# Kernel optimization log

Hardware: AMD Instinct MI355X
Metric: run time of the kernel (lower is better)

The kernel has to match this reference:

```python
import jax, jax.numpy as jnp
import numpy as np

B, C, D, H, W = 2, 128, 16, 16, 16

def setup_inputs() -> dict:
    key = jax.random.key(0)
    ks = jax.random.split(key, 7)
    s = 0.02
    return {
        "x": jax.random.normal(ks[0], (B, C, D, H, W), jnp.float32),
        "Wq": jax.random.normal(ks[1], (C, C), jnp.float32) * s,
        "bq": jax.random.normal(ks[2], (C,), jnp.float32) * s,
        "Wk": jax.random.normal(ks[3], (C, C), jnp.float32) * s,
        "bk": jax.random.normal(ks[4], (C,), jnp.float32) * s,
        "Wv": jax.random.normal(ks[5], (C, C), jnp.float32) * s,
        "bv": jax.random.normal(ks[6], (C,), jnp.float32) * s,
    }

def reference(x, Wq, bq, Wk, bk, Wv, bv):
    b, c, d, h, w = x.shape
    n = d * h * w
    xf = x.reshape(b, c, n)  # [B, C, N]
    # 1x1x1 Conv3d == per-voxel linear over channels
    q = jnp.einsum('oc,bcn->bon', Wq, xf) + bq[None, :, None]
    k = jnp.einsum('oc,bcn->bon', Wk, xf) + bk[None, :, None]
    v = jnp.einsum('oc,bcn->bon', Wv, xf) + bv[None, :, None]
    # energy[b,n,m] = sum_c q[b,c,n] * k[b,c,m]  (no scale, as in source)
    energy = jnp.einsum('bcn,bcm->bnm', q, k)
    attention = jax.nn.softmax(energy, axis=-1)
    # out[b,c,n] = sum_m v[b,c,m] * attention[b,n,m]
    out = jnp.einsum('bcm,bnm->bcn', v, attention)
    return out.reshape(b, c, d, h, w)
```

## Files before the change

### kernel.cpp

```cpp
#include <hip/hip_runtime.h>


typedef __bf16 bf16x8 __attribute__((ext_vector_type(8)));
typedef float  f32x4  __attribute__((ext_vector_type(4)));
typedef unsigned short ushort8 __attribute__((ext_vector_type(8)));
typedef unsigned short ushort4v __attribute__((ext_vector_type(4)));

#define LDP 136
#define LDV 72
#define LDO 133

constexpr int CB = 128;
constexpr int NB = 4096;
constexpr int BB = 2;

__device__ __forceinline__ unsigned short f2bf(float f) {
  union { float f; unsigned int i; } v; v.f = f;
  unsigned int x = v.i;
  return (unsigned short)((x + 0x7fffu + ((x >> 16) & 1u)) >> 16);
}
__device__ __forceinline__ bf16x8 ldfrag(const unsigned short* lds, int row, int koff, int ld) {
  return *(const bf16x8*)(lds + row * ld + koff);
}

__global__ __launch_bounds__(256) void qkv_proj_kernel(
    const float* __restrict__ x,
    const float* __restrict__ Wq, const float* __restrict__ bq,
    const float* __restrict__ Wk, const float* __restrict__ bk,
    const float* __restrict__ Wv, const float* __restrict__ bv,
    unsigned short* __restrict__ Qt, unsigned short* __restrict__ Kt,
    unsigned short* __restrict__ Vo)
{
  extern __shared__ __align__(16) char smem_raw[];
  unsigned short* xT = (unsigned short*)smem_raw;
  unsigned short* Wl = xT + 64 * LDP;

  const int b  = blockIdx.y;
  const int n0 = blockIdx.x * 64;
  const int m  = blockIdx.z;
  const int t  = threadIdx.x;
  const int lane = t & 63, w = t >> 6;
  const int l15 = lane & 15, quad = lane >> 4;

  const float* W = (m == 0) ? Wq : (m == 1) ? Wk : Wv;
  const float* bias_p = (m == 0) ? bq : (m == 1) ? bk : bv;

  for (int v = t; v < 2048; v += 256) {
    int c = v >> 4, i4 = v & 15;
    float4 d = *(const float4*)(x + (b * CB + c) * NB + n0 + i4 * 4);
    xT[(i4 * 4 + 0) * LDP + c] = f2bf(d.x);
    xT[(i4 * 4 + 1) * LDP + c] = f2bf(d.y);
    xT[(i4 * 4 + 2) * LDP + c] = f2bf(d.z);
    xT[(i4 * 4 + 3) * LDP + c] = f2bf(d.w);
  }
  for (int v = t; v < 4096; v += 256) {
    int o = v >> 5, c4 = v & 31;
    float4 d = *(const float4*)(W + o * 128 + c4 * 4);
    ushort4v u = {f2bf(d.x), f2bf(d.y), f2bf(d.z), f2bf(d.w)};
    *(ushort4v*)(Wl + o * LDP + c4 * 4) = u;
  }
  __syncthreads();

  if (m < 2) {
    f32x4 acc[8];
#pragma unroll
    for (int ct = 0; ct < 8; ct++) acc[ct] = (f32x4)0.0f;
#pragma unroll
    for (int ks = 0; ks < 4; ks++) {
      int koff = ks * 32 + quad * 8;
      bf16x8 a = ldfrag(xT, w * 16 + l15, koff, LDP);
#pragma unroll
      for (int ct = 0; ct < 8; ct++) {
        bf16x8 bb = ldfrag(Wl, ct * 16 + l15, koff, LDP);
        acc[ct] = __builtin_amdgcn_mfma_f32_16x16x32_bf16(a, bb, acc[ct], 0, 0, 0);
      }
    }
    unsigned short* O = (m == 0) ? Qt : Kt;
#pragma unroll
    for (int ct = 0; ct < 8; ct++) {
      int o = ct * 16 + l15;
      float bias = bias_p[o];
#pragma unroll
      for (int r = 0; r < 4; r++) {
        int i = w * 16 + quad * 4 + r;
        O[(b * NB + n0 + i) * CB + o] = f2bf(acc[ct][r] + bias);
      }
    }
  } else {
    f32x4 acc[2][4];
#pragma unroll
    for (int rr = 0; rr < 2; rr++)
#pragma unroll
      for (int ct = 0; ct < 4; ct++) acc[rr][ct] = (f32x4)0.0f;
#pragma unroll
    for (int ks = 0; ks < 4; ks++) {
      int koff = ks * 32 + quad * 8;
      bf16x8 a0 = ldfrag(Wl, (w * 2 + 0) * 16 + l15, koff, LDP);
      bf16x8 a1 = ldfrag(Wl, (w * 2 + 1) * 16 + l15, koff, LDP);
#pragma unroll
      for (int ct = 0; ct < 4; ct++) {
        bf16x8 bb = ldfrag(xT, ct * 16 + l15, koff, LDP);
        acc[0][ct] = __builtin_amdgcn_mfma_f32_16x16x32_bf16(a0, bb, acc[0][ct], 0, 0, 0);
        acc[1][ct] = __builtin_amdgcn_mfma_f32_16x16x32_bf16(a1, bb, acc[1][ct], 0, 0, 0);
      }
    }
#pragma unroll
    for (int rr = 0; rr < 2; rr++)
#pragma unroll
      for (int ct = 0; ct < 4; ct++)
#pragma unroll
        for (int r = 0; r < 4; r++) {
          int o = (w * 2 + rr) * 16 + quad * 4 + r;
          int i = ct * 16 + l15;
          Vo[(b * CB + o) * NB + n0 + i] = f2bf(acc[rr][ct][r] + bias_p[o]);
        }
  }
}

__global__ __launch_bounds__(512, 4) void attn_part_kernel(
    const unsigned short* __restrict__ Qt,
    const unsigned short* __restrict__ Kt,
    const unsigned short* __restrict__ Vo,
    float* __restrict__ Opart, float* __restrict__ Ll, int ksz)
{
  extern __shared__ __align__(16) char smem_raw[];
  unsigned short* Kl = (unsigned short*)smem_raw;
  unsigned short* Vl = Kl + 64 * LDP;
  unsigned short* Pl = Vl + 128 * LDV;

  const int b  = blockIdx.y;
  const int q0 = blockIdx.x * 128;
  const int s  = blockIdx.z;
  const int k_base = s * ksz;
  const int nit = ksz >> 6;
  const int t  = threadIdx.x;
  const int lane = t & 63, w = t >> 6;
  const int l15 = lane & 15, quad = lane >> 4;

  bf16x8 qf[4];
#pragma unroll
  for (int ks = 0; ks < 4; ks++)
    qf[ks] = *(const bf16x8*)(Qt + ((size_t)(b * NB + q0 + w * 16 + l15)) * CB +
                              ks * 32 + quad * 8);

  for (int v = t; v < 1024; v += 512) {
    int j = v >> 4, c8 = v & 15;
    *(ushort8*)(Kl + j * LDP + c8 * 8) =
        *(const ushort8*)(Kt + (size_t)(b * NB + k_base + j) * CB + c8 * 8);
  }
  for (int v = t; v < 1024; v += 512) {
    int c = v >> 3, j8 = v & 7;
    *(ushort8*)(Vl + c * LDV + j8 * 8) =
        *(const ushort8*)(Vo + (size_t)(b * CB + c) * NB + k_base + j8 * 8);
  }

  float lsum[4] = {0.0f, 0.0f, 0.0f, 0.0f};
  f32x4 o_acc[8];
#pragma unroll
  for (int tt = 0; tt < 8; tt++) o_acc[tt] = (f32x4)0.0f;

  __syncthreads();

  for (int it = 0; it < nit; it++) {
    ushort8 kr[2], vr[2];
    if (it + 1 < nit) {
      int m1 = k_base + (it + 1) * 64;
#pragma unroll
      for (int u = 0; u < 2; u++) {
        int v = t + u * 512;
        int j = v >> 4, c8 = v & 15;
        kr[u] = *(const ushort8*)(Kt + (size_t)(b * NB + m1 + j) * CB + c8 * 8);
      }
#pragma unroll
      for (int u = 0; u < 2; u++) {
        int v = t + u * 512;
        int c = v >> 3, j8 = v & 7;
        vr[u] = *(const ushort8*)(Vo + (size_t)(b * CB + c) * NB + m1 + j8 * 8);
      }
    }

    f32x4 sacc[4];
#pragma unroll
    for (int tt = 0; tt < 4; tt++) sacc[tt] = (f32x4)0.0f;
#pragma unroll
    for (int ks = 0; ks < 4; ks++) {
      int koff = ks * 32 + quad * 8;
#pragma unroll
      for (int tt = 0; tt < 4; tt++) {
        bf16x8 bb = ldfrag(Kl, tt * 16 + l15, koff, LDP);
        sacc[tt] = __builtin_amdgcn_mfma_f32_16x16x32_bf16(qf[ks], bb, sacc[tt], 0, 0, 0);
      }
    }

#pragma unroll
    for (int tt = 0; tt < 4; tt++) {
#pragma unroll
      for (int r = 0; r < 4; r++) {
        float p = __expf(sacc[tt][r]);
        sacc[tt][r] = p;
        lsum[r] += p;
        Pl[(w * 16 + quad * 4 + r) * LDV + tt * 16 + l15] = f2bf(p);
      }
    }
    asm volatile("s_waitcnt lgkmcnt(0)" ::: "memory");

#pragma unroll
    for (int ks = 0; ks < 2; ks++) {
      int koff = ks * 32 + quad * 8;
      bf16x8 a = ldfrag(Pl, w * 16 + l15, koff, LDV);
#pragma unroll
      for (int tt = 0; tt < 8; tt++) {
        bf16x8 bb = ldfrag(Vl, tt * 16 + l15, koff, LDV);
        o_acc[tt] = __builtin_amdgcn_mfma_f32_16x16x32_bf16(a, bb, o_acc[tt], 0, 0, 0);
      }
    }

    if (it + 1 < nit) {
      __syncthreads();
#pragma unroll
      for (int u = 0; u < 2; u++) {
        int v = t + u * 512;
        int j = v >> 4, c8 = v & 15;
        *(ushort8*)(Kl + j * LDP + c8 * 8) = kr[u];
      }
#pragma unroll
      for (int u = 0; u < 2; u++) {
        int v = t + u * 512;
        int c = v >> 3, j8 = v & 7;
        *(ushort8*)(Vl + c * LDV + j8 * 8) = vr[u];
      }
      __syncthreads();
    }
  }

#pragma unroll
  for (int r = 0; r < 4; r++) {
    lsum[r] += __shfl_xor(lsum[r], 1, 16);
    lsum[r] += __shfl_xor(lsum[r], 2, 16);
    lsum[r] += __shfl_xor(lsum[r], 4, 16);
    lsum[r] += __shfl_xor(lsum[r], 8, 16);
  }

  const size_t obase = ((size_t)(s * BB + b) * NB + q0) * CB;
#pragma unroll
  for (int tt = 0; tt < 8; tt++)
#pragma unroll
    for (int r = 0; r < 4; r++)
      Opart[obase + (size_t)(w * 16 + quad * 4 + r) * CB + tt * 16 + l15] = o_acc[tt][r];
  if (l15 == 0) {
    const size_t lbase = (size_t)(s * BB + b) * NB + q0 + w * 16;
#pragma unroll
    for (int r = 0; r < 4; r++) Ll[lbase + quad * 4 + r] = lsum[r];
  }
}

__global__ __launch_bounds__(256) void combine_kernel(
    const float* __restrict__ Opart, const float* __restrict__ Ll,
    float* __restrict__ out, int nsplit)
{
  extern __shared__ __align__(16) char smem_raw[];
  float* Olf = (float*)smem_raw;

  const int b  = blockIdx.y;
  const int n0 = blockIdx.x * 64;
  const int t  = threadIdx.x;
  const int i  = t >> 2;
  const int c0 = (t & 3) * 32;

  float L = 0.0f;
  for (int s = 0; s < nsplit; s++)
    L += Ll[(size_t)(s * BB + b) * NB + n0 + i];

  f32x4 acc[8];
#pragma unroll
  for (int u = 0; u < 8; u++) acc[u] = (f32x4)0.0f;
  for (int s = 0; s < nsplit; s++) {
    const float* src = Opart + ((size_t)(s * BB + b) * NB + n0 + i) * CB + c0;
#pragma unroll
    for (int u = 0; u < 8; u++) acc[u] += *(const f32x4*)(src + u * 4);
  }
  float invL = 1.0f / L;
#pragma unroll
  for (int u = 0; u < 8; u++) {
    acc[u] *= invL;
    *(f32x4*)(Olf + i * LDO + c0 + u * 4) = acc[u];
  }
  __syncthreads();

  for (int v = t; v < 2048; v += 256) {
    int c = v >> 4, i4 = v & 15;
    float4 d;
    d.x = Olf[(i4 * 4 + 0) * LDO + c];
    d.y = Olf[(i4 * 4 + 1) * LDO + c];
    d.z = Olf[(i4 * 4 + 2) * LDO + c];
    d.w = Olf[(i4 * 4 + 3) * LDO + c];
    *(float4*)(out + (size_t)(b * CB + c) * NB + n0 + i4 * 4) = d;
  }
}

extern "C" void kernel_launch(void* const* d_in, const int* in_sizes, int n_in,
                              void* d_out, int out_size, void* d_ws, size_t ws_size,
                              hipStream_t stream) {
  const float* x  = (const float*)d_in[0];
  const float* Wq = (const float*)d_in[1];
  const float* bq = (const float*)d_in[2];
  const float* Wk = (const float*)d_in[3];
  const float* bk = (const float*)d_in[4];
  const float* Wv = (const float*)d_in[5];
  const float* bv = (const float*)d_in[6];
  float* out = (float*)d_out;

  const size_t qkv_elems = (size_t)BB * NB * CB;
  unsigned short* Qt = (unsigned short*)d_ws;
  unsigned short* Kt = Qt + qkv_elems;
  unsigned short* Vo = Kt + qkv_elems;
  char* ws_tail = (char*)(Vo + qkv_elems);
  size_t tail_sz = ws_size - 3 * qkv_elems * sizeof(unsigned short);

  const size_t per_split = (size_t)BB * NB * CB * 4 + (size_t)BB * NB * 4;
  int nsplit = 8;
  while (nsplit > 1 && (size_t)nsplit * per_split > tail_sz) nsplit >>= 1;

  float* Opart = (float*)ws_tail;
  float* Ll    = Opart + (size_t)nsplit * BB * NB * CB;
  const int ksz = NB / nsplit;

  const int qkv_smem  = (64 * LDP + 128 * LDP) * 2;
  const int attn_smem = (64 * LDP + 128 * LDV + 128 * LDV) * 2;
  const int comb_smem = 64 * LDO * 4;

  qkv_proj_kernel<<<dim3(NB / 64, BB, 3), 256, qkv_smem, stream>>>(
      x, Wq, bq, Wk, bk, Wv, bv, Qt, Kt, Vo);
  attn_part_kernel<<<dim3(NB / 128, BB, nsplit), 512, attn_smem, stream>>>(
      Qt, Kt, Vo, Opart, Ll, ksz);
  combine_kernel<<<dim3(NB / 64, BB), 256, comb_smem, stream>>>(
      Opart, Ll, out, nsplit);
}
```

Baseline: 125.6 us.

## Use 32-row query tiles per wave, split combine over channels, native bf16 casts

The attention kernel now runs 4 waves of 256 threads, each handling two 16-row query subtiles. Every K/V fragment read from LDS therefore feeds two MFMAs, halving LDS traffic per FLOP, at the cost of more accumulator registers. The combine kernel is split into four channel groups so it launches four times as many blocks, with a smaller LDS transpose tile. Manual float-to-bf16 rounding is replaced with native __bf16 casts, which may lower to hardware conversion instructions.

```diff
diff --git a/kernel.cpp b/kernel.cpp
--- a/kernel.cpp
+++ b/kernel.cpp
@@ -2,24 +2,18 @@
 
 
 typedef __bf16 bf16x8 __attribute__((ext_vector_type(8)));
+typedef __bf16 bf16x4v __attribute__((ext_vector_type(4)));
 typedef float  f32x4  __attribute__((ext_vector_type(4)));
-typedef unsigned short ushort8 __attribute__((ext_vector_type(8)));
-typedef unsigned short ushort4v __attribute__((ext_vector_type(4)));
 
 #define LDP 136
 #define LDV 72
-#define LDO 133
+#define LDO 33
 
 constexpr int CB = 128;
 constexpr int NB = 4096;
 constexpr int BB = 2;
 
-__device__ __forceinline__ unsigned short f2bf(float f) {
-  union { float f; unsigned int i; } v; v.f = f;
-  unsigned int x = v.i;
-  return (unsigned short)((x + 0x7fffu + ((x >> 16) & 1u)) >> 16);
-}
-__device__ __forceinline__ bf16x8 ldfrag(const unsigned short* lds, int row, int koff, int ld) {
+__device__ __forceinline__ bf16x8 ldfrag(const __bf16* lds, int row, int koff, int ld) {
   return *(const bf16x8*)(lds + row * ld + koff);
 }
 
@@ -28,12 +22,11 @@
     const float* __restrict__ Wq, const float* __restrict__ bq,
     const float* __restrict__ Wk, const float* __restrict__ bk,
     const float* __restrict__ Wv, const float* __restrict__ bv,
-    unsigned short* __restrict__ Qt, unsigned short* __restrict__ Kt,
-    unsigned short* __restrict__ Vo)
+    __bf16* __restrict__ Qt, __bf16* __restrict__ Kt, __bf16* __restrict__ Vo)
 {
   extern __shared__ __align__(16) char smem_raw[];
-  unsigned short* xT = (unsigned short*)smem_raw;
-  unsigned short* Wl = xT + 64 * LDP;
+  __bf16* xT = (__bf16*)smem_raw;
+  __bf16* Wl = xT + 64 * LDP;
 
   const int b  = blockIdx.y;
   const int n0 = blockIdx.x * 64;
@@ -48,16 +41,16 @@
   for (int v = t; v < 2048; v += 256) {
     int c = v >> 4, i4 = v & 15;
     float4 d = *(const float4*)(x + (b * CB + c) * NB + n0 + i4 * 4);
-    xT[(i4 * 4 + 0) * LDP + c] = f2bf(d.x);
-    xT[(i4 * 4 + 1) * LDP + c] = f2bf(d.y);
-    xT[(i4 * 4 + 2) * LDP + c] = f2bf(d.z);
-    xT[(i4 * 4 + 3) * LDP + c] = f2bf(d.w);
+    xT[(i4 * 4 + 0) * LDP + c] = (__bf16)d.x;
+    xT[(i4 * 4 + 1) * LDP + c] = (__bf16)d.y;
+    xT[(i4 * 4 + 2) * LDP + c] = (__bf16)d.z;
+    xT[(i4 * 4 + 3) * LDP + c] = (__bf16)d.w;
   }
   for (int v = t; v < 4096; v += 256) {
     int o = v >> 5, c4 = v & 31;
     float4 d = *(const float4*)(W + o * 128 + c4 * 4);
-    ushort4v u = {f2bf(d.x), f2bf(d.y), f2bf(d.z), f2bf(d.w)};
-    *(ushort4v*)(Wl + o * LDP + c4 * 4) = u;
+    bf16x4v u = {(__bf16)d.x, (__bf16)d.y, (__bf16)d.z, (__bf16)d.w};
+    *(bf16x4v*)(Wl + o * LDP + c4 * 4) = u;
   }
   __syncthreads();
 
@@ -75,7 +68,7 @@
         acc[ct] = __builtin_amdgcn_mfma_f32_16x16x32_bf16(a, bb, acc[ct], 0, 0, 0);
       }
     }
-    unsigned short* O = (m == 0) ? Qt : Kt;
+    __bf16* O = (m == 0) ? Qt : Kt;
 #pragma unroll
     for (int ct = 0; ct < 8; ct++) {
       int o = ct * 16 + l15;
@@ -83,7 +76,7 @@
 #pragma unroll
       for (int r = 0; r < 4; r++) {
         int i = w * 16 + quad * 4 + r;
-        O[(b * NB + n0 + i) * CB + o] = f2bf(acc[ct][r] + bias);
+        O[(b * NB + n0 + i) * CB + o] = (__bf16)(acc[ct][r] + bias);
       }
     }
   } else {
@@ -112,21 +105,21 @@
         for (int r = 0; r < 4; r++) {
           int o = (w * 2 + rr) * 16 + quad * 4 + r;
           int i = ct * 16 + l15;
-          Vo[(b * CB + o) * NB + n0 + i] = f2bf(acc[rr][ct][r] + bias_p[o]);
+          Vo[(b * CB + o) * NB + n0 + i] = (__bf16)(acc[rr][ct][r] + bias_p[o]);
         }
   }
 }
 
-__global__ __launch_bounds__(512, 4) void attn_part_kernel(
-    const unsigned short* __restrict__ Qt,
-    const unsigned short* __restrict__ Kt,
-    const unsigned short* __restrict__ Vo,
+__global__ __launch_bounds__(256, 2) void attn_part_kernel(
+    const __bf16* __restrict__ Qt,
+    const __bf16* __restrict__ Kt,
+    const __bf16* __restrict__ Vo,
     float* __restrict__ Opart, float* __restrict__ Ll, int ksz)
 {
   extern __shared__ __align__(16) char smem_raw[];
-  unsigned short* Kl = (unsigned short*)smem_raw;
-  unsigned short* Vl = Kl + 64 * LDP;
-  unsigned short* Pl = Vl + 128 * LDV;
+  __bf16* Kl = (__bf16*)smem_raw;
+  __bf16* Vl = Kl + 64 * LDP;
+  __bf16* Pl = Vl + 128 * LDV;
 
   const int b  = blockIdx.y;
   const int q0 = blockIdx.x * 128;
@@ -136,121 +129,143 @@
   const int t  = threadIdx.x;
   const int lane = t & 63, w = t >> 6;
   const int l15 = lane & 15, quad = lane >> 4;
-
-  bf16x8 qf[4];
-#pragma unroll
-  for (int ks = 0; ks < 4; ks++)
-    qf[ks] = *(const bf16x8*)(Qt + ((size_t)(b * NB + q0 + w * 16 + l15)) * CB +
-                              ks * 32 + quad * 8);
-
-  for (int v = t; v < 1024; v += 512) {
+  const int row0 = w * 32;
+
+  bf16x8 qf[2][4];
+#pragma unroll
+  for (int st = 0; st < 2; st++)
+#pragma unroll
+    for (int ks = 0; ks < 4; ks++)
+      qf[st][ks] = *(const bf16x8*)(Qt +
+          (size_t)(b * NB + q0 + row0 + st * 16 + l15) * CB + ks * 32 + quad * 8);
+
+#pragma unroll
+  for (int u = 0; u < 4; u++) {
+    int v = t + u * 256;
     int j = v >> 4, c8 = v & 15;
-    *(ushort8*)(Kl + j * LDP + c8 * 8) =
-        *(const ushort8*)(Kt + (size_t)(b * NB + k_base + j) * CB + c8 * 8);
-  }
-  for (int v = t; v < 1024; v += 512) {
+    *(bf16x8*)(Kl + j * LDP + c8 * 8) =
+        *(const bf16x8*)(Kt + (size_t)(b * NB + k_base + j) * CB + c8 * 8);
+  }
+#pragma unroll
+  for (int u = 0; u < 4; u++) {
+    int v = t + u * 256;
     int c = v >> 3, j8 = v & 7;
-    *(ushort8*)(Vl + c * LDV + j8 * 8) =
-        *(const ushort8*)(Vo + (size_t)(b * CB + c) * NB + k_base + j8 * 8);
-  }
-
-  float lsum[4] = {0.0f, 0.0f, 0.0f, 0.0f};
-  f32x4 o_acc[8];
-#pragma unroll
-  for (int tt = 0; tt < 8; tt++) o_acc[tt] = (f32x4)0.0f;
+    *(bf16x8*)(Vl + c * LDV + j8 * 8) =
+        *(const bf16x8*)(Vo + (size_t)(b * CB + c) * NB + k_base + j8 * 8);
+  }
+
+  float lsum[2][4] = {{0, 0, 0, 0}, {0, 0, 0, 0}};
+  f32x4 o_acc[2][8];
+#pragma unroll
+  for (int st = 0; st < 2; st++)
+#pragma unroll
+    for (int tt = 0; tt < 8; tt++) o_acc[st][tt] = (f32x4)0.0f;
 
   __syncthreads();
 
   for (int it = 0; it < nit; it++) {
-    ushort8 kr[2], vr[2];
+    bf16x8 kr[4], vr[4];
     if (it + 1 < nit) {
       int m1 = k_base + (it + 1) * 64;
 #pragma unroll
-      for (int u = 0; u < 2; u++) {
-        int v = t + u * 512;
+      for (int u = 0; u < 4; u++) {
+        int v = t + u * 256;
         int j = v >> 4, c8 = v & 15;
-        kr[u] = *(const ushort8*)(Kt + (size_t)(b * NB + m1 + j) * CB + c8 * 8);
-      }
-#pragma unroll
-      for (int u = 0; u < 2; u++) {
-        int v = t + u * 512;
+        kr[u] = *(const bf16x8*)(Kt + (size_t)(b * NB + m1 + j) * CB + c8 * 8);
+      }
+#pragma unroll
+      for (int u = 0; u < 4; u++) {
+        int v = t + u * 256;
         int c = v >> 3, j8 = v & 7;
-        vr[u] = *(const ushort8*)(Vo + (size_t)(b * CB + c) * NB + m1 + j8 * 8);
-      }
-    }
-
-    f32x4 sacc[4];
-#pragma unroll
-    for (int tt = 0; tt < 4; tt++) sacc[tt] = (f32x4)0.0f;
+        vr[u] = *(const bf16x8*)(Vo + (size_t)(b * CB + c) * NB + m1 + j8 * 8);
+      }
+    }
+
+    f32x4 sacc[2][4];
+#pragma unroll
+    for (int st = 0; st < 2; st++)
+#pragma unroll
+      for (int tt = 0; tt < 4; tt++) sacc[st][tt] = (f32x4)0.0f;
 #pragma unroll
     for (int ks = 0; ks < 4; ks++) {
       int koff = ks * 32 + quad * 8;
 #pragma unroll
       for (int tt = 0; tt < 4; tt++) {
         bf16x8 bb = ldfrag(Kl, tt * 16 + l15, koff, LDP);
-        sacc[tt] = __builtin_amdgcn_mfma_f32_16x16x32_bf16(qf[ks], bb, sacc[tt], 0, 0, 0);
-      }
-    }
-
-#pragma unroll
-    for (int tt = 0; tt < 4; tt++) {
-#pragma unroll
-      for (int r = 0; r < 4; r++) {
-        float p = __expf(sacc[tt][r]);
-        sacc[tt][r] = p;
-        lsum[r] += p;
-        Pl[(w * 16 + quad * 4 + r) * LDV + tt * 16 + l15] = f2bf(p);
-      }
-    }
+        sacc[0][tt] = __builtin_amdgcn_mfma_f32_16x16x32_bf16(qf[0][ks], bb, sacc[0][tt], 0, 0, 0);
+        sacc[1][tt] = __builtin_amdgcn_mfma_f32_16x16x32_bf16(qf[1][ks], bb, sacc[1][tt], 0, 0, 0);
+      }
+    }
+
+#pragma unroll
+    for (int st = 0; st < 2; st++)
+#pragma unroll
+      for (int tt = 0; tt < 4; tt++)
+#pragma unroll
+        for (int r = 0; r < 4; r++) {
+          float p = __expf(sacc[st][tt][r]);
+          lsum[st][r] += p;
+          Pl[(row0 + st * 16 + quad * 4 + r) * LDV + tt * 16 + l15] = (__bf16)p;
+        }
     asm volatile("s_waitcnt lgkmcnt(0)" ::: "memory");
 
 #pragma unroll
     for (int ks = 0; ks < 2; ks++) {
       int koff = ks * 32 + quad * 8;
-      bf16x8 a = ldfrag(Pl, w * 16 + l15, koff, LDV);
+      bf16x8 a0 = ldfrag(Pl, row0 + l15, koff, LDV);
+      bf16x8 a1 = ldfrag(Pl, row0 + 16 + l15, koff, LDV);
 #pragma unroll
       for (int tt = 0; tt < 8; tt++) {
         bf16x8 bb = ldfrag(Vl, tt * 16 + l15, koff, LDV);
-        o_acc[tt] = __builtin_amdgcn_mfma_f32_16x16x32_bf16(a, bb, o_acc[tt], 0, 0, 0);
+        o_acc[0][tt] = __builtin_amdgcn_mfma_f32_16x16x32_bf16(a0, bb, o_acc[0][tt], 0, 0, 0);
+        o_acc[1][tt] = __builtin_amdgcn_mfma_f32_16x16x32_bf16(a1, bb, o_acc[1][tt], 0, 0, 0);
       }
     }
 
     if (it + 1 < nit) {
       __syncthreads();
 #pragma unroll
-      for (int u = 0; u < 2; u++) {
-        int v = t + u * 512;
+      for (int u = 0; u < 4; u++) {
+        int v = t + u * 256;
         int j = v >> 4, c8 = v & 15;
-        *(ushort8*)(Kl + j * LDP + c8 * 8) = kr[u];
-      }
-#pragma unroll
-      for (int u = 0; u < 2; u++) {
-        int v = t + u * 512;
+        *(bf16x8*)(Kl + j * LDP + c8 * 8) = kr[u];
+      }
+#pragma unroll
+      for (int u = 0; u < 4; u++) {
+        int v = t + u * 256;
         int c = v >> 3, j8 = v & 7;
-        *(ushort8*)(Vl + c * LDV + j8 * 8) = vr[u];
+        *(bf16x8*)(Vl + c * LDV + j8 * 8) = vr[u];
       }
       __syncthreads();
     }
   }
 
 #pragma unroll
-  for (int r = 0; r < 4; r++) {
-    lsum[r] += __shfl_xor(lsum[r], 1, 16);
-    lsum[r] += __shfl_xor(lsum[r], 2, 16);
-    lsum[r] += __shfl_xor(lsum[r], 4, 16);
-    lsum[r] += __shfl_xor(lsum[r], 8, 16);
-  }
+  for (int st = 0; st < 2; st++)
+#pragma unroll
+    for (int r = 0; r < 4; r++) {
+      lsum[st][r] += __shfl_xor(lsum[st][r], 1, 16);
+      lsum[st][r] += __shfl_xor(lsum[st][r], 2, 16);
+      lsum[st][r] += __shfl_xor(lsum[st][r], 4, 16);
+      lsum[st][r] += __shfl_xor(lsum[st][r], 8, 16);
+    }
 
   const size_t obase = ((size_t)(s * BB + b) * NB + q0) * CB;
 #pragma unroll
-  for (int tt = 0; tt < 8; tt++)
-#pragma unroll
-    for (int r = 0; r < 4; r++)
-      Opart[obase + (size_t)(w * 16 + quad * 4 + r) * CB + tt * 16 + l15] = o_acc[tt][r];
+  for (int st = 0; st < 2; st++)
+#pragma unroll
+    for (int tt = 0; tt < 8; tt++)
+#pragma unroll
+      for (int r = 0; r < 4; r++)
+        Opart[obase + (size_t)(row0 + st * 16 + quad * 4 + r) * CB + tt * 16 + l15] =
+            o_acc[st][tt][r];
   if (l15 == 0) {
-    const size_t lbase = (size_t)(s * BB + b) * NB + q0 + w * 16;
-#pragma unroll
-    for (int r = 0; r < 4; r++) Ll[lbase + quad * 4 + r] = lsum[r];
+    const size_t lbase = (size_t)(s * BB + b) * NB + q0 + row0;
+#pragma unroll
+    for (int st = 0; st < 2; st++)
+#pragma unroll
+      for (int r = 0; r < 4; r++)
+        Ll[lbase + st * 16 + quad * 4 + r] = lsum[st][r];
   }
 }
 
@@ -263,38 +278,39 @@
 
   const int b  = blockIdx.y;
   const int n0 = blockIdx.x * 64;
+  const int c0 = blockIdx.z * 32;
   const int t  = threadIdx.x;
   const int i  = t >> 2;
-  const int c0 = (t & 3) * 32;
+  const int cc = (t & 3) * 8;
 
   float L = 0.0f;
   for (int s = 0; s < nsplit; s++)
     L += Ll[(size_t)(s * BB + b) * NB + n0 + i];
 
-  f32x4 acc[8];
-#pragma unroll
-  for (int u = 0; u < 8; u++) acc[u] = (f32x4)0.0f;
+  f32x4 acc[2];
+  acc[0] = (f32x4)0.0f; acc[1] = (f32x4)0.0f;
   for (int s = 0; s < nsplit; s++) {
-    const float* src = Opart + ((size_t)(s * BB + b) * NB + n0 + i) * CB + c0;
-#pragma unroll
-    for (int u = 0; u < 8; u++) acc[u] += *(const f32x4*)(src + u * 4);
+    const float* src = Opart + ((size_t)(s * BB + b) * NB + n0 + i) * CB + c0 + cc;
+    acc[0] += *(const f32x4*)(src);
+    acc[1] += *(const f32x4*)(src + 4);
   }
   float invL = 1.0f / L;
 #pragma unroll
-  for (int u = 0; u < 8; u++) {
+  for (int u = 0; u < 2; u++) {
     acc[u] *= invL;
-    *(f32x4*)(Olf + i * LDO + c0 + u * 4) = acc[u];
+#pragma unroll
+    for (int e = 0; e < 4; e++) Olf[i * LDO + cc + u * 4 + e] = acc[u][e];
   }
   __syncthreads();
 
-  for (int v = t; v < 2048; v += 256) {
+  for (int v = t; v < 512; v += 256) {
     int c = v >> 4, i4 = v & 15;
     float4 d;
     d.x = Olf[(i4 * 4 + 0) * LDO + c];
     d.y = Olf[(i4 * 4 + 1) * LDO + c];
     d.z = Olf[(i4 * 4 + 2) * LDO + c];
     d.w = Olf[(i4 * 4 + 3) * LDO + c];
-    *(float4*)(out + (size_t)(b * CB + c) * NB + n0 + i4 * 4) = d;
+    *(float4*)(out + (size_t)(b * CB + c0 + c) * NB + n0 + i4 * 4) = d;
   }
 }
 
@@ -311,11 +327,11 @@
   float* out = (float*)d_out;
 
   const size_t qkv_elems = (size_t)BB * NB * CB;
-  unsigned short* Qt = (unsigned short*)d_ws;
-  unsigned short* Kt = Qt + qkv_elems;
-  unsigned short* Vo = Kt + qkv_elems;
+  __bf16* Qt = (__bf16*)d_ws;
+  __bf16* Kt = Qt + qkv_elems;
+  __bf16* Vo = Kt + qkv_elems;
   char* ws_tail = (char*)(Vo + qkv_elems);
-  size_t tail_sz = ws_size - 3 * qkv_elems * sizeof(unsigned short);
+  size_t tail_sz = ws_size - 3 * qkv_elems * sizeof(__bf16);
 
   const size_t per_split = (size_t)BB * NB * CB * 4 + (size_t)BB * NB * 4;
   int nsplit = 8;
@@ -331,8 +347,8 @@
 
   qkv_proj_kernel<<<dim3(NB / 64, BB, 3), 256, qkv_smem, stream>>>(
       x, Wq, bq, Wk, bk, Wv, bv, Qt, Kt, Vo);
-  attn_part_kernel<<<dim3(NB / 128, BB, nsplit), 512, attn_smem, stream>>>(
+  attn_part_kernel<<<dim3(NB / 128, BB, nsplit), 256, attn_smem, stream>>>(
       Qt, Kt, Vo, Opart, Ll, ksz);
-  combine_kernel<<<dim3(NB / 64, BB), 256, comb_smem, stream>>>(
+  combine_kernel<<<dim3(NB / 64, BB, 4), 256, comb_smem, stream>>>(
       Opart, Ll, out, nsplit);
 }
```

Result: faster. 118.5 us (-5.6%).
